# Kernel optimization log

Measured on AMD Instinct MI355X. Metric: run time of the kernel, lower is better.

Reference implementation:

```python
import jax, jax.numpy as jnp
import numpy as np
from jax import lax

N = 4667      # num vertices (hardcoded in Spatial_Attention_layer)
B = 4         # batch
T = 8         # raw timesteps; (T-2)*3 == 18 after TimeBlock + concat
C_IN = 2      # input features
TP = 18       # concatenated timesteps
HID = 16      # TimeBlock out channels / PCN fc width
N_ROOTS = 500
BRANCH = 2
DEPTH = 3


def _build_tree():
    # Static stand-in for the P/roots/s2rDic dict-based trajectory tree.
    rng = np.random.RandomState(42)
    roots = rng.choice(N, N_ROOTS, replace=False)
    path_node = [int(r) for r in roots]
    levels = []
    prev = list(range(N_ROOTS))
    for _ in range(DEPTH):
        p_idx, c_idx, pn, cn, nxt = [], [], [], [], []
        for pi in prev:
            kids = rng.choice(N, BRANCH, replace=False)
            for c in kids:
                ci = len(path_node)
                path_node.append(int(c))
                p_idx.append(pi); c_idx.append(ci)
                pn.append(path_node[pi]); cn.append(int(c))
                nxt.append(ci)
        levels.append((np.array(p_idx), np.array(c_idx), np.array(pn), np.array(cn)))
        prev = nxt
    leaf_idx = np.array(prev)
    leaf_node = np.array([path_node[i] for i in prev])
    return np.asarray(roots), levels, leaf_idx, leaf_node, len(path_node)

ROOTS, LEVELS, LEAF_IDX, LEAF_NODES, NUM_PATHS = _build_tree()
ROOT_PATH_IDX = np.arange(N_ROOTS)


def setup_inputs() -> dict:
    key = jax.random.key(0)
    ks = jax.random.split(key, 16)
    f = jnp.float32
    rn = lambda k, s: 0.1 * jax.random.normal(k, s, f)
    return {
        "X": jax.random.normal(ks[0], (B, N, T, C_IN), f),
        "X_daily": jax.random.normal(ks[1], (B, N, T, C_IN), f),
        "X_weekly": jax.random.normal(ks[2], (B, N, T, C_IN), f),
        "mask": jnp.zeros((1,), jnp.int32),  # unused in forward (as in source)
        "conv1_w": rn(ks[3], (HID, C_IN, 1, 3)),
        "conv1_b": rn(ks[4], (HID,)),
        "conv2_w": rn(ks[5], (HID, C_IN, 1, 3)),
        "conv2_b": rn(ks[6], (HID,)),
        "W1": rn(ks[7], (HID,)),
        "W2": rn(ks[8], (TP, HID)),
        "W3": rn(ks[9], (TP,)),
        "bs": rn(ks[10], (1, N, N)),
        "Vs": rn(ks[11], (N, N)),
        "fc_w": rn(ks[12], (HID, HID)),
        "fc_b": rn(ks[13], (HID,)),
    }


def reference(X, X_daily, X_weekly, mask, conv1_w, conv1_b, conv2_w, conv2_b,
              W1, W2, W3, bs, Vs, fc_w, fc_b):
    dn = ("NCHW", "OIHW", "NCHW")

    def time_block(Xin):
        # [B,N,T,C] -> [B,C,N,T] -> GLU conv over time -> [B,N,T-2,HID]
        Xp = jnp.transpose(Xin, (0, 3, 1, 2))
        c1 = lax.conv_general_dilated(Xp, conv1_w, (1, 1), "VALID", dimension_numbers=dn) + conv1_b[None, :, None, None]
        c2 = lax.conv_general_dilated(Xp, conv2_w, (1, 1), "VALID", dimension_numbers=dn) + conv2_b[None, :, None, None]
        return jnp.transpose(c1 * jax.nn.sigmoid(c2), (0, 2, 3, 1))

    x = jnp.concatenate([time_block(X), time_block(X_daily), time_block(X_weekly)], axis=2)  # [B,N,18,16]

    # spatial attention
    lhs = jnp.einsum("bnt,tc->bnc", jnp.einsum("bntc,c->bnt", x, W1), W2)   # [B,N,16]
    rhs = jnp.einsum("t,bntc->bnc", W3, x)                                    # [B,N,16]
    product = jnp.einsum("bnc,bmc->bnm", lhs, rhs)                            # [B,N,N]
    S = jnp.einsum("nm,bmk->bnk", Vs, jax.nn.sigmoid(product + bs))           # [B,N,N]
    A = jax.nn.softmax(S, axis=1)

    # PCN tree propagation: h_child = fc(h_parent) * A[:, p, c] + x[c]
    xn = jnp.transpose(x, (1, 0, 2, 3))  # [N,B,18,16]
    H = jnp.zeros((NUM_PATHS, B, TP, HID), x.dtype)
    H = H.at[ROOT_PATH_IDX].set(xn[ROOTS])
    for p_idx, c_idx, pn, cn in LEVELS:
        hp = H[p_idx]                                   # [E,B,18,16]
        a = jnp.transpose(A[:, pn, cn])                 # [E,B]
        hc = (jnp.einsum("ebtc,dc->ebtd", hp, fc_w) + fc_b) * a[:, :, None, None] + xn[cn]
        H = H.at[c_idx].set(hc)

    # mean-pool leaf paths per terminal node; fall back to x for nodes w/o leaves
    leaf_h = H[LEAF_IDX]
    sums = jax.ops.segment_sum(leaf_h, LEAF_NODES, num_segments=N)
    counts = jax.ops.segment_sum(jnp.ones((LEAF_NODES.shape[0],), x.dtype), LEAF_NODES, num_segments=N)
    has_leaf = (counts > 0)[:, None, None, None]
    out_n = jnp.where(has_leaf, sums / jnp.maximum(counts, 1.0)[:, None, None, None], xn)
    return jnp.transpose(out_n, (1, 0, 2, 3))  # [B,N,18,16]
```

## Files before the change

kernel.cpp:

```cpp
#include <hip/hip_runtime.h>
#include <stdint.h>
#include <string.h>

#define NV      4667
#define BB      4
#define TT      8
#define TPX     18
#define HID     16
#define NROOTS  500
#define NPATHS  7500
#define NEDGES  7000
#define NLEAF   4000
#define NP2     4864
#define LDKQ    5120

typedef __bf16 bf16;
typedef bf16  bf16x4 __attribute__((ext_vector_type(4)));
typedef int   i32x4v __attribute__((ext_vector_type(4)));
typedef int   i32x16 __attribute__((ext_vector_type(16)));
typedef const void __attribute__((address_space(1))) gvoid;
typedef void       __attribute__((address_space(3))) svoid;

struct MT19937 {
    uint32_t mt[624]; int pos;
    void seed(uint32_t s) {
        for (int i = 0; i < 624; ++i) { mt[i] = s; s = 1812433253u * (s ^ (s >> 30)) + (uint32_t)i + 1u; }
        pos = 624;
    }
    uint32_t next() {
        if (pos >= 624) {
            for (int i = 0; i < 624; ++i) {
                uint32_t y = (mt[i] & 0x80000000u) | (mt[(i + 1) % 624] & 0x7fffffffu);
                uint32_t v = mt[(i + 397) % 624] ^ (y >> 1);
                if (y & 1u) v ^= 0x9908b0dfu;
                mt[i] = v;
            }
            pos = 0;
        }
        uint32_t y = mt[pos++];
        y ^= y >> 11; y ^= (y << 7) & 0x9d2c5680u; y ^= (y << 15) & 0xefc60000u; y ^= y >> 18;
        return y;
    }
    uint32_t interval(uint32_t mx) {
        if (!mx) return 0;
        uint32_t mask = mx;
        mask |= mask >> 1; mask |= mask >> 2; mask |= mask >> 4; mask |= mask >> 8; mask |= mask >> 16;
        uint32_t v;
        do { v = next() & mask; } while (v > mx);
        return v;
    }
};

struct TreeBlob {
    int path_node[NPATHS];
    int leaf_start[NV + 1];
    int leaf_path[NLEAF];
};

static void build_tree_host(TreeBlob* tb) {
    MT19937 rng; rng.seed(42);
    static int perm[NV];
    auto choice_take = [&](int* out, int k) {
        for (int i = 0; i < NV; ++i) perm[i] = i;
        for (int i = NV - 1; i >= 1; --i) {
            int j = (int)rng.interval((uint32_t)i);
            int t = perm[i]; perm[i] = perm[j]; perm[j] = t;
        }
        for (int i = 0; i < k; ++i) out[i] = perm[i];
    };
    int np_ = 0;
    int roots[NROOTS];
    choice_take(roots, NROOTS);
    for (int i = 0; i < NROOTS; ++i) tb->path_node[np_++] = roots[i];
    int prev_cnt = NROOTS;
    for (int lvl = 0; lvl < 3; ++lvl) {
        int kids[2];
        for (int p = 0; p < prev_cnt; ++p) {
            choice_take(kids, 2);
            tb->path_node[np_++] = kids[0];
            tb->path_node[np_++] = kids[1];
        }
        prev_cnt *= 2;
    }
    static int cnt[NV], cur[NV];
    memset(cnt, 0, sizeof(cnt));
    for (int l = 0; l < NLEAF; ++l) cnt[tb->path_node[3500 + l]]++;
    tb->leaf_start[0] = 0;
    for (int n = 0; n < NV; ++n) tb->leaf_start[n + 1] = tb->leaf_start[n] + cnt[n];
    for (int n = 0; n < NV; ++n) cur[n] = tb->leaf_start[n];
    for (int l = 0; l < NLEAF; ++l) {
        int n = tb->path_node[3500 + l];
        tb->leaf_path[cur[n]++] = 3500 + l;
    }
}

static TreeBlob* get_pinned_tree() {
    static TreeBlob* p = [] {
        TreeBlob* q = nullptr;
        if (hipHostMalloc((void**)&q, sizeof(TreeBlob), 0) != hipSuccess || !q) {
            static TreeBlob fallback;
            q = &fallback;
        }
        build_tree_host(q);
        return q;
    }();
    return p;
}

__global__ void k_timeblock(const float* __restrict__ X, const float* __restrict__ Xd,
                            const float* __restrict__ Xw,
                            const float* __restrict__ w1, const float* __restrict__ b1,
                            const float* __restrict__ w2, const float* __restrict__ b2,
                            float* __restrict__ x) {
    int idx = blockIdx.x * 256 + threadIdx.x;
    if (idx >= BB * NV * 18) return;
    int t = idx % 6;
    int g = (idx / 6) % 3;
    int n = (idx / 18) % NV;
    int b = idx / (18 * NV);
    const float* Xg = (g == 0) ? X : (g == 1) ? Xd : Xw;
    const float* p = Xg + (((size_t)b * NV + n) * TT + t) * 2;
    float v[6];
#pragma unroll
    for (int kk = 0; kk < 3; ++kk) { v[kk * 2 + 0] = p[kk * 2 + 0]; v[kk * 2 + 1] = p[kk * 2 + 1]; }
    float* xo = x + (((size_t)b * NV + n) * TPX + (g * 6 + t)) * HID;
#pragma unroll
    for (int o = 0; o < 16; ++o) {
        float c1 = b1[o], c2 = b2[o];
#pragma unroll
        for (int ci = 0; ci < 2; ++ci)
#pragma unroll
            for (int kk = 0; kk < 3; ++kk) {
                float xv = v[kk * 2 + ci];
                c1 += xv * w1[(o * 2 + ci) * 3 + kk];
                c2 += xv * w2[(o * 2 + ci) * 3 + kk];
            }
        xo[o] = c1 * (1.0f / (1.0f + __expf(-c2)));
    }
}

__global__ void k_lhsrhs(const float* __restrict__ x, const float* __restrict__ W1,
                         const float* __restrict__ W2, const float* __restrict__ W3,
                         float* __restrict__ lhs, float* __restrict__ rhs) {
    int idx = blockIdx.x * 256 + threadIdx.x;
    if (idx >= BB * NV) return;
    const float* xp = x + (size_t)idx * TPX * HID;
    float l[16], r[16];
#pragma unroll
    for (int c = 0; c < 16; ++c) { l[c] = 0.f; r[c] = 0.f; }
    for (int t = 0; t < TPX; ++t) {
        float xt = 0.f, w3 = W3[t];
#pragma unroll
        for (int c = 0; c < 16; ++c) { float xv = xp[t * 16 + c]; xt += xv * W1[c]; r[c] += w3 * xv; }
#pragma unroll
        for (int c = 0; c < 16; ++c) l[c] += xt * W2[t * 16 + c];
    }
    float* lo = lhs + (size_t)idx * 16;
    float* ro = rhs + (size_t)idx * 16;
#pragma unroll
    for (int c = 0; c < 16; ++c) { lo[c] = l[c]; ro[c] = r[c]; }
}

__global__ __launch_bounds__(256)
void k_vsq(const float* __restrict__ Vs, int8_t* __restrict__ Vq,
           float* __restrict__ sA, float* __restrict__ c0) {
    int n = blockIdx.x;
    int t = threadIdx.x;
    int8_t* row_out = Vq + (size_t)n * LDKQ;
    if (n >= NV) {
        for (int m = t * 4; m < LDKQ; m += 1024) *(int*)(row_out + m) = 0;
        if (t == 0) { sA[n] = 0.f; c0[n] = 0.f; }
        return;
    }
    const float* row = Vs + (size_t)n * NV;
    float v[20];
    float mx = 0.f;
#pragma unroll
    for (int i = 0; i < 20; ++i) {
        int m = t + i * 256;
        v[i] = (m < NV) ? row[m] : 0.f;
        mx = fmaxf(mx, fabsf(v[i]));
    }
#pragma unroll
    for (int o = 32; o; o >>= 1) mx = fmaxf(mx, __shfl_xor(mx, o));
    __shared__ float wred[4];
    __shared__ int ired[4];
    if ((t & 63) == 0) wred[t >> 6] = mx;
    __syncthreads();
    mx = fmaxf(fmaxf(wred[0], wred[1]), fmaxf(wred[2], wred[3]));
    mx = fmaxf(mx, 1e-30f);
    float inv = 127.f / mx;
    int qs = 0;
#pragma unroll
    for (int i = 0; i < 20; ++i) {
        int q = (int)rintf(v[i] * inv);
        qs += q;
        row_out[t + i * 256] = (int8_t)q;
    }
#pragma unroll
    for (int o = 32; o; o >>= 1) qs += __shfl_xor(qs, o);
    if ((t & 63) == 0) ired[t >> 6] = qs;
    __syncthreads();
    if (t == 0) {
        int tot = ired[0] + ired[1] + ired[2] + ired[3];
        sA[n] = mx / 32258.f;
        c0[n] = mx * (float)tot / 254.f;
    }
}

__global__ __launch_bounds__(256)
void k_sig(const float* __restrict__ lhs, const float* __restrict__ rhs,
           const float* __restrict__ bs, int8_t* __restrict__ Sq) {
    int m0 = blockIdx.x * 256;
    int k0 = blockIdx.y * 64;
    __shared__ bf16 bss[64 * 260];
    int t = threadIdx.x;

    for (int i = t; i < 256 * 64; i += 256) {
        int row = i >> 6, col = i & 63;
        int mg = m0 + row, kg = k0 + col;
        float v = (mg < NV && kg < NV) ? bs[(size_t)mg * NV + kg] : 0.f;
        bss[col * 260 + row] = (bf16)v;
    }
    __syncthreads();

    int ml = t & 63, kc = t >> 6;
    int mbase = m0 + ml * 4;

    for (int b = 0; b < BB; ++b) {
        float lv[4][16];
#pragma unroll
        for (int r = 0; r < 4; ++r) {
            int mg = mbase + r;
            if (mg < NV) {
                const float4* lp = (const float4*)&lhs[((size_t)b * NV + mg) * 16];
#pragma unroll
                for (int q = 0; q < 4; ++q) {
                    float4 f = lp[q];
                    lv[r][q * 4 + 0] = f.x; lv[r][q * 4 + 1] = f.y;
                    lv[r][q * 4 + 2] = f.z; lv[r][q * 4 + 3] = f.w;
                }
            } else {
#pragma unroll
                for (int c = 0; c < 16; ++c) lv[r][c] = 0.f;
            }
        }
#pragma unroll
        for (int kk = 0; kk < 16; ++kk) {
            int kl = kc * 16 + kk;
            int kg = k0 + kl;
            bool kvalid = (kg < NV);
            float rsv[16];
            if (kvalid) {
                const float4* rp = (const float4*)&rhs[((size_t)b * NV + kg) * 16];
#pragma unroll
                for (int q = 0; q < 4; ++q) {
                    float4 f = rp[q];
                    rsv[q * 4 + 0] = f.x; rsv[q * 4 + 1] = f.y;
                    rsv[q * 4 + 2] = f.z; rsv[q * 4 + 3] = f.w;
                }
            } else {
#pragma unroll
                for (int c = 0; c < 16; ++c) rsv[c] = 0.f;
            }
            bf16x4 bv = *(const bf16x4*)&bss[kl * 260 + ml * 4];
            int pack = 0;
#pragma unroll
            for (int r = 0; r < 4; ++r) {
                float dot = 0.f;
#pragma unroll
                for (int c = 0; c < 16; ++c) dot += lv[r][c] * rsv[c];
                float pv = dot + (float)bv[r];
                float s = 1.0f / (1.0f + __expf(-pv));
                int q = 0;
                if (kvalid && (mbase + r) < NV) q = (int)rintf(254.f * (s - 0.5f));
                pack |= (q & 0xff) << (8 * r);
            }
            *(int*)&Sq[((size_t)b * NP2 + kg) * LDKQ + mbase] = pack;
        }
    }
}

#define STAGE4(dstoff, gptr, kt) { \
    const int8_t* _g = (gptr) + (size_t)(kt) * 128; \
    __builtin_amdgcn_global_load_lds((gvoid*)(_g),                     (svoid*)(sb + (dstoff) + dst0), 16, 0, 0); \
    __builtin_amdgcn_global_load_lds((gvoid*)(_g + (size_t)64 * LDKQ), (svoid*)(sb + (dstoff) + dst0 + 8192), 16, 0, 0); \
    __builtin_amdgcn_global_load_lds((gvoid*)(_g + (size_t)128 * LDKQ),(svoid*)(sb + (dstoff) + dst0 + 16384), 16, 0, 0); \
    __builtin_amdgcn_global_load_lds((gvoid*)(_g + (size_t)192 * LDKQ),(svoid*)(sb + (dstoff) + dst0 + 24576), 16, 0, 0); }

#define READ_G(ar, br, RB, K0) { \
    _Pragma("unroll") for (int mf = 0; mf < 4; ++mf) { \
        ar[mf][0] = *(const i32x4v*)((RB) + abase + mf * 4096 + colks[K0]); \
        ar[mf][1] = *(const i32x4v*)((RB) + abase + mf * 4096 + colks[K0 + 1]); } \
    _Pragma("unroll") for (int nf = 0; nf < 2; ++nf) { \
        br[nf][0] = *(const i32x4v*)((RB) + bbase + nf * 4096 + colks[K0]); \
        br[nf][1] = *(const i32x4v*)((RB) + bbase + nf * 4096 + colks[K0 + 1]); } }

#define MMA_G(ar, br) { \
    __builtin_amdgcn_s_setprio(1); \
    _Pragma("unroll") for (int kk = 0; kk < 2; ++kk) \
    _Pragma("unroll") for (int mf = 0; mf < 4; ++mf) \
    _Pragma("unroll") for (int nf = 0; nf < 2; ++nf) \
        acc[mf][nf] = __builtin_amdgcn_mfma_i32_32x32x32_i8(ar[mf][kk], br[nf][kk], acc[mf][nf], 0, 0, 0); \
    __builtin_amdgcn_s_setprio(0); }

#define WINDOW(RB, SB, TSTAGE) { \
    char* sb = (SB); \
    STAGE4(0, gA, TSTAGE); \
    STAGE4(32768, gB, TSTAGE); \
    READ_G(a0, b0, RB, 0); \
    READ_G(a1, b1, RB, 2); \
    MMA_G(a0, b0); \
    MMA_G(a1, b1); \
    asm volatile("s_waitcnt vmcnt(0)" ::: "memory"); \
    __builtin_amdgcn_s_barrier(); }

__global__ __launch_bounds__(512, 2)
void k_gemm32(const int8_t* __restrict__ Vq, const int8_t* __restrict__ Sq,
              const float* __restrict__ sA, const float* __restrict__ c0,
              float* __restrict__ colsum) {
    extern __shared__ char ldsb[];

    int orig = blockIdx.x;
    int xcd = orig & 7, lin = orig >> 3;
    int wg = (xcd < 4) ? xcd * 181 + lin : 724 + (xcd - 4) * 180 + lin;
    int bi = wg % 19;
    int bk = (wg / 19) % 19;
    int bb = wg / 361;

    int t = threadIdx.x;
    int lane = t & 63, wv = t >> 6;
    int wr = wv >> 2, wc = wv & 3;
    int l31 = lane & 31, hi = lane >> 5;
    int key = (lane & 7) << 4;
    int colks[4];
#pragma unroll
    for (int ks = 0; ks < 4; ++ks) colks[ks] = (ks * 32 + hi * 16) ^ key;
    int abase = wr * 16384 + l31 * 128;
    int bbase = 32768 + wc * 8192 + l31 * 128;

    int rl0 = t >> 3;
    int csw = ((t & 7) << 4) ^ ((rl0 & 7) << 4);
    const int8_t* gA = Vq + ((size_t)(bi * 256) + rl0) * LDKQ + csw;
    const int8_t* gB = Sq + ((size_t)bb * NP2 + (size_t)bk * 256 + rl0) * LDKQ + csw;
    int dst0 = t * 16;

    i32x16 acc[4][2];
#pragma unroll
    for (int i = 0; i < 4; ++i)
#pragma unroll
        for (int j = 0; j < 2; ++j)
#pragma unroll
            for (int r = 0; r < 16; ++r) acc[i][j][r] = 0;

    i32x4v a0[4][2], a1[4][2], b0[2][2], b1[2][2];

    {
        char* sb = ldsb;
        STAGE4(0, gA, 0);
        STAGE4(32768, gB, 0);
    }
    asm volatile("s_waitcnt vmcnt(0)" ::: "memory");
    __builtin_amdgcn_s_barrier();

    for (int i = 0; i < 19; ++i) {
        WINDOW(ldsb,         ldsb + 65536, 2 * i + 1);
        WINDOW(ldsb + 65536, ldsb,         2 * i + 2);
    }

#pragma unroll
    for (int nf = 0; nf < 2; ++nf) {
        int col = bk * 256 + wc * 64 + nf * 32 + l31;
        float csum = 0.f;
#pragma unroll
        for (int mf = 0; mf < 4; ++mf) {
            int rowb = bi * 256 + wr * 128 + mf * 32 + 4 * hi;
#pragma unroll
            for (int g = 0; g < 4; ++g) {
                int rg = rowb + 8 * g;
                float4 sa4 = *(const float4*)&sA[rg];
                float4 c04 = *(const float4*)&c0[rg];
                float sar[4] = {sa4.x, sa4.y, sa4.z, sa4.w};
                float c0r[4] = {c04.x, c04.y, c04.z, c04.w};
#pragma unroll
                for (int r = 0; r < 4; ++r) {
                    float S = sar[r] * (float)acc[mf][nf][g * 4 + r] + c0r[r];
                    csum += ((rg + r) < NV && col < NV) ? __expf(S) : 0.f;
                }
            }
        }
        csum += __shfl_xor(csum, 32);
        if (lane < 32 && col < NV) atomicAdd(&colsum[(size_t)bb * NV + col], csum);
    }
}

__global__ void k_edge(const int8_t* __restrict__ Vq, const int8_t* __restrict__ Sq,
                       const float* __restrict__ sA, const float* __restrict__ c0,
                       const float* __restrict__ colsum, const int* __restrict__ path_node,
                       float* __restrict__ a_edge) {
    int g = blockIdx.x;
    int b = threadIdx.x >> 6;
    int lane = threadIdx.x & 63;
    int e, pbase, cbase;
    if (g < 1000)      { e = g;        pbase = 0;    cbase = 500;  }
    else if (g < 3000) { e = g - 1000; pbase = 500;  cbase = 1500; }
    else               { e = g - 3000; pbase = 1500; cbase = 3500; }
    int pn = path_node[pbase + (e >> 1)];
    int cn = path_node[cbase + e];
    const int8_t* va = Vq + (size_t)pn * LDKQ;
    const int8_t* vb = Sq + ((size_t)b * NP2 + cn) * LDKQ;
    int acc = 0;
    for (int i = lane * 16; i < LDKQ; i += 1024) {
        i32x4v a4 = *(const i32x4v*)(va + i);
        i32x4v b4 = *(const i32x4v*)(vb + i);
#pragma unroll
        for (int w = 0; w < 4; ++w) {
            int aw = a4[w], bw = b4[w];
#pragma unroll
            for (int q = 0; q < 4; ++q)
                acc += (int)(int8_t)(aw >> (8 * q)) * (int)(int8_t)(bw >> (8 * q));
        }
    }
#pragma unroll
    for (int o = 32; o; o >>= 1) acc += __shfl_xor(acc, o);
    if (lane == 0) {
        float S = sA[pn] * (float)acc + c0[pn];
        a_edge[(size_t)g * BB + b] = __expf(S) / colsum[(size_t)b * NV + cn];
    }
}

__global__ void k_root(const float* __restrict__ x, const int* __restrict__ path_node,
                       float* __restrict__ H) {
    int idx = blockIdx.x * 256 + threadIdx.x;
    if (idx >= NROOTS * BB * 288) return;
    int d = idx % 288;
    int b = (idx / 288) % BB;
    int p = idx / (288 * BB);
    int n = path_node[p];
    H[((size_t)p * BB + b) * 288 + d] = x[((size_t)b * NV + n) * 288 + d];
}

__global__ void k_level(const float* __restrict__ x, const int* __restrict__ path_node,
                        const float* __restrict__ fcw, const float* __restrict__ fcb,
                        const float* __restrict__ a_edge, float* __restrict__ H,
                        int E, int pbase, int cbase, int gbase) {
    int idx = blockIdx.x * 256 + threadIdx.x;
    if (idx >= E * BB * 288) return;
    int d = idx & 15;
    int t = (idx >> 4) % TPX;
    int b = (idx / (16 * TPX)) % BB;
    int e = idx / (16 * TPX * BB);
    int pp = pbase + (e >> 1);
    int cp = cbase + e;
    const float* hp = &H[(((size_t)pp * BB + b) * TPX + t) * HID];
    float acc = fcb[d];
#pragma unroll
    for (int c = 0; c < 16; ++c) acc += hp[c] * fcw[d * 16 + c];
    float a = a_edge[(size_t)(gbase + e) * BB + b];
    int cn = path_node[cp];
    float xv = x[(((size_t)b * NV + cn) * TPX + t) * HID + d];
    H[(((size_t)cp * BB + b) * TPX + t) * HID + d] = acc * a + xv;
}

__global__ void k_pool(const float* __restrict__ x, const float* __restrict__ H,
                       const int* __restrict__ leaf_start, const int* __restrict__ leaf_path,
                       float* __restrict__ out) {
    int n = blockIdx.x;
    int s = leaf_start[n], epos = leaf_start[n + 1];
    int cnt = epos - s;
    for (int idx = threadIdx.x; idx < BB * 288; idx += 256) {
        int b = idx / 288, d = idx % 288;
        float v;
        if (cnt == 0) {
            v = x[((size_t)b * NV + n) * 288 + d];
        } else {
            float sum = 0.f;
            for (int l = s; l < epos; ++l) {
                int p = leaf_path[l];
                sum += H[((size_t)p * BB + b) * 288 + d];
            }
            v = sum / (float)cnt;
        }
        out[((size_t)b * NV + n) * 288 + d] = v;
    }
}

extern "C" void kernel_launch(void* const* d_in, const int* in_sizes, int n_in,
                              void* d_out, int out_size, void* d_ws, size_t ws_size,
                              hipStream_t stream) {
    const float* X   = (const float*)d_in[0];
    const float* Xd  = (const float*)d_in[1];
    const float* Xw  = (const float*)d_in[2];
    const float* c1w = (const float*)d_in[4];
    const float* c1b = (const float*)d_in[5];
    const float* c2w = (const float*)d_in[6];
    const float* c2b = (const float*)d_in[7];
    const float* W1  = (const float*)d_in[8];
    const float* W2  = (const float*)d_in[9];
    const float* W3  = (const float*)d_in[10];
    const float* bs  = (const float*)d_in[11];
    const float* Vs  = (const float*)d_in[12];
    const float* fcw = (const float*)d_in[13];
    const float* fcb = (const float*)d_in[14];
    float* out = (float*)d_out;

    TreeBlob* pinned = get_pinned_tree();

    char* w = (char*)d_ws;
    auto alloc = [&](size_t bytes) { char* p = w; w += (bytes + 255) & ~(size_t)255; return p; };
    float*  x      = (float*)alloc((size_t)BB * NV * 288 * 4);
    float*  lhs    = (float*)alloc((size_t)BB * NV * 16 * 4);
    float*  rhs    = (float*)alloc((size_t)BB * NV * 16 * 4);
    float*  colsum = (float*)alloc((size_t)BB * NV * 4);
    float*  aedge  = (float*)alloc((size_t)NEDGES * BB * 4);
    float*  H      = (float*)alloc((size_t)NPATHS * BB * 288 * 4);
    float*  sAr    = (float*)alloc((size_t)NP2 * 4);
    float*  c0r    = (float*)alloc((size_t)NP2 * 4);
    int*    dtree  = (int*)alloc(sizeof(TreeBlob));
    int8_t* Vq     = (int8_t*)alloc((size_t)NP2 * LDKQ);
    int8_t* Sq     = (int8_t*)alloc((size_t)BB * NP2 * LDKQ);

    int* d_path   = dtree;
    int* d_lstart = dtree + NPATHS;
    int* d_lpath  = d_lstart + (NV + 1);

    hipFuncSetAttribute((const void*)k_gemm32, hipFuncAttributeMaxDynamicSharedMemorySize, 131072);

    hipMemcpyAsync(dtree, pinned, sizeof(TreeBlob), hipMemcpyHostToDevice, stream);
    hipMemsetAsync(colsum, 0, (size_t)BB * NV * 4, stream);

    k_timeblock<<<(BB * NV * 18 + 255) / 256, 256, 0, stream>>>(X, Xd, Xw, c1w, c1b, c2w, c2b, x);
    k_lhsrhs<<<(BB * NV + 255) / 256, 256, 0, stream>>>(x, W1, W2, W3, lhs, rhs);
    k_vsq<<<NP2, 256, 0, stream>>>(Vs, Vq, sAr, c0r);
    dim3 sgrid(LDKQ / 256, NP2 / 64);
    k_sig<<<sgrid, 256, 0, stream>>>(lhs, rhs, bs, Sq);
    k_gemm32<<<19 * 19 * BB, 512, 131072, stream>>>(Vq, Sq, sAr, c0r, colsum);
    k_edge<<<NEDGES, 256, 0, stream>>>(Vq, Sq, sAr, c0r, colsum, d_path, aedge);
    k_root<<<(NROOTS * BB * 288 + 255) / 256, 256, 0, stream>>>(x, d_path, H);
    k_level<<<(1000 * BB * 288 + 255) / 256, 256, 0, stream>>>(x, d_path, fcw, fcb, aedge, H, 1000, 0, 500, 0);
    k_level<<<(2000 * BB * 288 + 255) / 256, 256, 0, stream>>>(x, d_path, fcw, fcb, aedge, H, 2000, 500, 1500, 1000);
    k_level<<<(4000 * BB * 288 + 255) / 256, 256, 0, stream>>>(x, d_path, fcw, fcb, aedge, H, 4000, 1500, 3500, 3000);
    k_pool<<<NV, 256, 0, stream>>>(x, H, d_lstart, d_lpath, out);
}
```

Baseline: 856.2 us.

## Interleave LDS reads, global-to-LDS staging and MFMA per half-window with barriers

Restructures the int8 GEMM main loop so each double-buffered window is split into two halves. Each half reads one pair of K fragments, issues part of the next tile's global-to-LDS staging, then runs the MFMAs, with barriers between phases. Using one register fragment set instead of two lowers register pressure and spreads memory traffic across the MFMA work. The cost is more barriers per iteration, which adds synchronization stalls and may reduce overlap.

New measurement: 856.9 us. About the same (+0.1%).

```diff
diff --git a/kernel.cpp b/kernel.cpp
--- a/kernel.cpp
+++ b/kernel.cpp
@@ -281,39 +281,35 @@
     }
 }
 
+#define BUF1    65536
+#define AOFF    0
+#define BOFF    32768
+
+#define BARRIER() __builtin_amdgcn_s_barrier()
+#define VM0()    asm volatile("s_waitcnt vmcnt(0)" ::: "memory")
+
 #define STAGE4(dstoff, gptr, kt) { \
     const int8_t* _g = (gptr) + (size_t)(kt) * 128; \
-    __builtin_amdgcn_global_load_lds((gvoid*)(_g),                     (svoid*)(sb + (dstoff) + dst0), 16, 0, 0); \
-    __builtin_amdgcn_global_load_lds((gvoid*)(_g + (size_t)64 * LDKQ), (svoid*)(sb + (dstoff) + dst0 + 8192), 16, 0, 0); \
-    __builtin_amdgcn_global_load_lds((gvoid*)(_g + (size_t)128 * LDKQ),(svoid*)(sb + (dstoff) + dst0 + 16384), 16, 0, 0); \
-    __builtin_amdgcn_global_load_lds((gvoid*)(_g + (size_t)192 * LDKQ),(svoid*)(sb + (dstoff) + dst0 + 24576), 16, 0, 0); }
-
-#define READ_G(ar, br, RB, K0) { \
+    __builtin_amdgcn_global_load_lds((gvoid*)(_g),                      (svoid*)(ldsb + (dstoff) + dst0), 16, 0, 0); \
+    __builtin_amdgcn_global_load_lds((gvoid*)(_g + (size_t)64 * LDKQ),  (svoid*)(ldsb + (dstoff) + dst0 + 8192), 16, 0, 0); \
+    __builtin_amdgcn_global_load_lds((gvoid*)(_g + (size_t)128 * LDKQ), (svoid*)(ldsb + (dstoff) + dst0 + 16384), 16, 0, 0); \
+    __builtin_amdgcn_global_load_lds((gvoid*)(_g + (size_t)192 * LDKQ), (svoid*)(ldsb + (dstoff) + dst0 + 24576), 16, 0, 0); }
+
+#define READF(BUFOFF, KS0) { \
     _Pragma("unroll") for (int mf = 0; mf < 4; ++mf) { \
-        ar[mf][0] = *(const i32x4v*)((RB) + abase + mf * 4096 + colks[K0]); \
-        ar[mf][1] = *(const i32x4v*)((RB) + abase + mf * 4096 + colks[K0 + 1]); } \
+        a[mf][0] = *(const i32x4v*)(ldsb + (BUFOFF) + abase + mf * 4096 + colks[KS0]); \
+        a[mf][1] = *(const i32x4v*)(ldsb + (BUFOFF) + abase + mf * 4096 + colks[(KS0) + 1]); } \
     _Pragma("unroll") for (int nf = 0; nf < 2; ++nf) { \
-        br[nf][0] = *(const i32x4v*)((RB) + bbase + nf * 4096 + colks[K0]); \
-        br[nf][1] = *(const i32x4v*)((RB) + bbase + nf * 4096 + colks[K0 + 1]); } }
-
-#define MMA_G(ar, br) { \
+        b[nf][0] = *(const i32x4v*)(ldsb + (BUFOFF) + bbase + nf * 4096 + colks[KS0]); \
+        b[nf][1] = *(const i32x4v*)(ldsb + (BUFOFF) + bbase + nf * 4096 + colks[(KS0) + 1]); } }
+
+#define MMAF() { \
     __builtin_amdgcn_s_setprio(1); \
     _Pragma("unroll") for (int kk = 0; kk < 2; ++kk) \
     _Pragma("unroll") for (int mf = 0; mf < 4; ++mf) \
     _Pragma("unroll") for (int nf = 0; nf < 2; ++nf) \
-        acc[mf][nf] = __builtin_amdgcn_mfma_i32_32x32x32_i8(ar[mf][kk], br[nf][kk], acc[mf][nf], 0, 0, 0); \
+        acc[mf][nf] = __builtin_amdgcn_mfma_i32_32x32x32_i8(a[mf][kk], b[nf][kk], acc[mf][nf], 0, 0, 0); \
     __builtin_amdgcn_s_setprio(0); }
-
-#define WINDOW(RB, SB, TSTAGE) { \
-    char* sb = (SB); \
-    STAGE4(0, gA, TSTAGE); \
-    STAGE4(32768, gB, TSTAGE); \
-    READ_G(a0, b0, RB, 0); \
-    READ_G(a1, b1, RB, 2); \
-    MMA_G(a0, b0); \
-    MMA_G(a1, b1); \
-    asm volatile("s_waitcnt vmcnt(0)" ::: "memory"); \
-    __builtin_amdgcn_s_barrier(); }
 
 __global__ __launch_bounds__(512, 2)
 void k_gemm32(const int8_t* __restrict__ Vq, const int8_t* __restrict__ Sq,
@@ -336,8 +332,8 @@
     int colks[4];
 #pragma unroll
     for (int ks = 0; ks < 4; ++ks) colks[ks] = (ks * 32 + hi * 16) ^ key;
-    int abase = wr * 16384 + l31 * 128;
-    int bbase = 32768 + wc * 8192 + l31 * 128;
+    int abase = AOFF + wr * 16384 + l31 * 128;
+    int bbase = BOFF + wc * 8192 + l31 * 128;
 
     int rl0 = t >> 3;
     int csw = ((t & 7) << 4) ^ ((rl0 & 7) << 4);
@@ -353,19 +349,37 @@
 #pragma unroll
             for (int r = 0; r < 16; ++r) acc[i][j][r] = 0;
 
-    i32x4v a0[4][2], a1[4][2], b0[2][2], b1[2][2];
-
-    {
-        char* sb = ldsb;
-        STAGE4(0, gA, 0);
-        STAGE4(32768, gB, 0);
-    }
-    asm volatile("s_waitcnt vmcnt(0)" ::: "memory");
-    __builtin_amdgcn_s_barrier();
+    i32x4v a[4][2], b[2][2];
+
+    STAGE4(AOFF, gA, 0);
+    STAGE4(BOFF, gB, 0);
+    VM0();
+    BARRIER();
 
     for (int i = 0; i < 19; ++i) {
-        WINDOW(ldsb,         ldsb + 65536, 2 * i + 1);
-        WINDOW(ldsb + 65536, ldsb,         2 * i + 2);
+        int t1 = 2 * i + 1, t2 = 2 * i + 2;
+        READF(0, 0);
+        STAGE4(BUF1 + AOFF, gA, t1);
+        BARRIER();
+        MMAF();
+        BARRIER();
+        READF(0, 2);
+        STAGE4(BUF1 + BOFF, gB, t1);
+        BARRIER();
+        MMAF();
+        VM0();
+        BARRIER();
+        READF(BUF1, 0);
+        STAGE4(AOFF, gA, t2);
+        BARRIER();
+        MMAF();
+        BARRIER();
+        READF(BUF1, 2);
+        STAGE4(BOFF, gB, t2);
+        BARRIER();
+        MMAF();
+        VM0();
+        BARRIER();
     }
 
 #pragma unroll
```
